# Kernel tuning notes

Hardware: AMD Instinct MI355X
Metric: run time of the kernel (lower is better)

Reference implementation:

```python
import jax, jax.numpy as jnp
import numpy as np

N_NEURONS = 50000
N_BKG = 100
N_SYN_BASIS = 5
N_EDGES = 500000
BATCH = 1
SEQ_T = 250
BKG_RATE_PROB = 0.25  # bkg_firing_rate(250) * 0.001


def setup_inputs() -> dict:
    key = jax.random.key(0)
    k_w, k_tau, k_sp, k_r, k_c = jax.random.split(key, 5)
    weights = jax.random.normal(k_w, (N_EDGES,), dtype=jnp.float32)
    tau_syn = jax.random.uniform(k_tau, (N_EDGES, N_SYN_BASIS), dtype=jnp.float32)
    # Bernoulli background spikes, shape [B*T, n_bkg_units]
    spikes = (jax.random.uniform(k_sp, (BATCH * SEQ_T, N_BKG)) < BKG_RATE_PROB).astype(jnp.float32)
    rows = jax.random.randint(k_r, (N_EDGES,), 0, N_NEURONS, dtype=jnp.int32)
    cols = jax.random.randint(k_c, (N_EDGES,), 0, N_BKG, dtype=jnp.int32)
    return {"weights": weights, "tau_syn": tau_syn, "spikes": spikes,
            "rows": rows, "cols": cols}


def reference(weights, tau_syn, spikes, rows, cols):
    # Per-receptor edge values: weights[e] * tau_syn[e, r]  -> [E, R]
    vals = weights[:, None] * tau_syn
    # Densify the (identical-structure) sparse matrix once for all receptors;
    # duplicate (row, col) indices accumulate, matching tf.sparse semantics
    # used through sparse_dense_matmul. W: [N, K, R]
    W = jnp.zeros((N_NEURONS, N_BKG, N_SYN_BASIS), dtype=spikes.dtype).at[rows, cols].add(vals)
    # i_receptor[r] = sparse_w_in @ spikes.T -> stacked [R, N, BT];
    # tf.transpose reverses axes -> [BT, N, R]; fused here as one einsum.
    out = jnp.einsum('nkr,bk->bnr', W, spikes)  # [BT, N, R]
    return out.reshape(BATCH, SEQ_T, N_NEURONS * N_SYN_BASIS)
```

## Files before the change

### kernel.cpp

```cpp
#include <hip/hip_runtime.h>


#define N_NEURONS 50000
#define N_BKG     100
#define N_SYN     5
#define N_EDGES   500000
#define SEQ_T     250
#define NCOL      (N_NEURONS * N_SYN)
#define RPB       16
#define NBINS     (N_NEURONS / RPB)
#define NPART     8
#define CAP_P     64
#define RECS_BIN  (NPART * CAP_P)
#define CPADF     80
#define BCOLS     80
#define STRIDE_J  37

#define LDS_BYTES 32000

#define WS_COUNT_OFF 0
#define WS_SPB_OFF   131072
#define WS_REC_OFF   262144

typedef __attribute__((ext_vector_type(8))) short bf16x8;
typedef __attribute__((ext_vector_type(4))) float f32x4;

__device__ inline unsigned short bf16_rne(float f) {
    unsigned u = __builtin_bit_cast(unsigned, f);
    u += 0x7FFFu + ((u >> 16) & 1u);
    return (unsigned short)(u >> 16);
}
__device__ inline float bf16_up(unsigned hw) {
    return __builtin_bit_cast(float, hw << 16);
}

__global__ __launch_bounds__(256) void bucket_kernel(
        const float* __restrict__ weights,
        const float* __restrict__ tau,
        const int*   __restrict__ rows,
        const int*   __restrict__ cols,
        const float* __restrict__ spikes,
        unsigned* __restrict__ count,
        uint4* __restrict__ rec,
        bf16x8* __restrict__ spbf) {
    int gid = blockIdx.x * 256 + threadIdx.x;
    if (gid < 4096) {
        int lane = gid & 63;
        int kk   = (gid >> 6) & 3;
        int nt   = gid >> 8;
        int t    = nt * 16 + (lane & 15);
        int k0   = kk * 32 + (lane >> 4) * 8;
        bf16x8 v;
#pragma unroll
        for (int i = 0; i < 8; ++i) {
            float s = 0.f;
            if (t < SEQ_T && (k0 + i) < N_BKG)
                s = spikes[t * N_BKG + k0 + i];
            v[i] = (short)bf16_rne(s);
        }
        spbf[gid] = v;
    }
    if (gid >= N_EDGES) return;
    int row = rows[gid];
    int col = cols[gid];
    float w = weights[gid];
    const float* tp = tau + (size_t)gid * N_SYN;
    int bin  = row >> 4;
    int part = blockIdx.x & (NPART - 1);
    unsigned slot = atomicAdd(&count[part * NBINS + bin], 1u);
    if (slot >= CAP_P) return;
    uint4 r;
    r.x = ((unsigned)col << 4) | (unsigned)(row & 15);
    r.y = (unsigned)bf16_rne(w * tp[0]) | ((unsigned)bf16_rne(w * tp[1]) << 16);
    r.z = (unsigned)bf16_rne(w * tp[2]) | ((unsigned)bf16_rne(w * tp[3]) << 16);
    r.w = (unsigned)bf16_rne(w * tp[4]);
    rec[(size_t)bin * RECS_BIN + part * CAP_P + slot] = r;
}

__global__ __launch_bounds__(256, 4) void fused_kernel(
        const unsigned* __restrict__ count,
        const uint4* __restrict__ rec,
        const bf16x8* __restrict__ spbf,
        float* __restrict__ out) {
    __shared__ __align__(16) char lds[LDS_BYTES];
    float* slice = (float*)lds;

    const int tid = threadIdx.x;
    const int l   = tid & 63;
    const int wv  = tid >> 6;
    const int lc  = l & 15;
    const int lq  = l >> 4;

    const int orig = blockIdx.x;
    const int xcd  = orig & 7;
    const int j    = orig >> 3;
    const int qx   = (xcd < 5) ? 391 : 390;
    const int base = (xcd < 5) ? xcd * 391 : 5 * 391 + (xcd - 5) * 390;
    const int bin  = base + (j * STRIDE_J) % qx;

    const uint4* rbin = rec + (size_t)bin * RECS_BIN;
    unsigned cntA = count[wv * NBINS + bin];
    unsigned cntB = count[(4 + wv) * NBINS + bin];
    if (cntA > CAP_P) cntA = CAP_P;
    if (cntB > CAP_P) cntB = CAP_P;
    uint4 ra = rbin[wv * CAP_P + l];
    uint4 rb = rbin[(4 + wv) * CAP_P + l];
    bool havea = (unsigned)l < cntA;
    bool haveb = (unsigned)l < cntB;

    {
        f32x4* s4 = (f32x4*)lds;
        f32x4 z = (f32x4){0.f, 0.f, 0.f, 0.f};
#pragma unroll
        for (int jj = 0; jj < 8; ++jj) {
            int i = tid + jj * 256;
            if (i < 2000) s4[i] = z;
        }
    }
    __syncthreads();

    if (havea) {
        float* bp = &slice[(ra.x >> 4) * CPADF + (ra.x & 15u) * N_SYN];
        atomicAdd(bp + 0, bf16_up(ra.y & 0xFFFFu));
        atomicAdd(bp + 1, bf16_up(ra.y >> 16));
        atomicAdd(bp + 2, bf16_up(ra.z & 0xFFFFu));
        atomicAdd(bp + 3, bf16_up(ra.z >> 16));
        atomicAdd(bp + 4, bf16_up(ra.w & 0xFFFFu));
    }
    if (haveb) {
        float* bp = &slice[(rb.x >> 4) * CPADF + (rb.x & 15u) * N_SYN];
        atomicAdd(bp + 0, bf16_up(rb.y & 0xFFFFu));
        atomicAdd(bp + 1, bf16_up(rb.y >> 16));
        atomicAdd(bp + 2, bf16_up(rb.z & 0xFFFFu));
        atomicAdd(bp + 3, bf16_up(rb.z >> 16));
        atomicAdd(bp + 4, bf16_up(rb.w & 0xFFFFu));
    }
    __syncthreads();

    bf16x8 hi[5];
#pragma unroll
    for (int jj = 0; jj < 5; ++jj) {
        int m  = tid + jj * 256;
        int c  = m % BCOLS;
        int kb = m / BCOLS;
#pragma unroll
        for (int i = 0; i < 8; ++i) {
            int k = kb * 8 + i;
            float v = (k < N_BKG) ? slice[k * CPADF + c] : 0.f;
            hi[jj][i] = (short)bf16_rne(v);
        }
    }
    __syncthreads();
#pragma unroll
    for (int jj = 0; jj < 5; ++jj) {
        int m  = tid + jj * 256;
        int c  = m % BCOLS;
        int kb = m / BCOLS;
        unsigned bo = (unsigned)(((c << 8) + (kb << 4)) ^ ((c & 7) << 4));
        *(bf16x8*)(lds + bo) = hi[jj];
    }

    bf16x8 bs[4][4];
#pragma unroll
    for (int n = 0; n < 4; ++n)
#pragma unroll
        for (int kk = 0; kk < 4; ++kk)
            bs[n][kk] = spbf[((wv * 4 + n) * 4 + kk) * 64 + l];
    __syncthreads();

    const size_t cb = (size_t)bin * BCOLS;
#pragma unroll
    for (int m = 0; m < 5; ++m) {
        f32x4 acc[4];
#pragma unroll
        for (int n = 0; n < 4; ++n)
            acc[n] = (f32x4){0.f, 0.f, 0.f, 0.f};

        int c = m * 16 + lc;
#pragma unroll
        for (int kk = 0; kk < 4; ++kk) {
            int bor = (((c << 8) + (kk << 6) + (lq << 4)) ^ ((c & 7) << 4));
            bf16x8 ah = *(const bf16x8*)(lds + bor);
#pragma unroll
            for (int n = 0; n < 4; ++n)
                acc[n] = __builtin_amdgcn_mfma_f32_16x16x32_bf16(
                             ah, bs[n][kk], acc[n], 0, 0, 0);
        }
        size_t cs = cb + m * 16 + lq * 4;
#pragma unroll
        for (int n = 0; n < 4; ++n) {
            int t = (wv * 4 + n) * 16 + lc;
            if (t < SEQ_T)
                *(f32x4*)(out + (size_t)t * NCOL + cs) = acc[n];
        }
    }
}

extern "C" void kernel_launch(void* const* d_in, const int* in_sizes, int n_in,
                              void* d_out, int out_size, void* d_ws, size_t ws_size,
                              hipStream_t stream) {
    const float* weights = (const float*)d_in[0];
    const float* tau     = (const float*)d_in[1];
    const float* spikes  = (const float*)d_in[2];
    const int*   rows    = (const int*)d_in[3];
    const int*   cols    = (const int*)d_in[4];
    float* out = (float*)d_out;

    char* ws = (char*)d_ws;
    unsigned* count = (unsigned*)(ws + WS_COUNT_OFF);
    bf16x8*   spbf  = (bf16x8*)(ws + WS_SPB_OFF);
    uint4*    rec   = (uint4*)(ws + WS_REC_OFF);

    hipMemsetAsync(count, 0, NPART * NBINS * sizeof(unsigned), stream);

    int eblocks = (N_EDGES + 255) / 256;
    bucket_kernel<<<eblocks, 256, 0, stream>>>(weights, tau, rows, cols, spikes,
                                               count, rec, spbf);

    fused_kernel<<<NBINS, 256, 0, stream>>>(count, rec, spbf, out);
}
```

Before: 112.6 us.

## Process two edges per thread, drop LDS bounds checks, pair M-tiles in MMA loop

The bucketing kernel now handles two edges per thread and launches half as many blocks. In the fused kernel, LDS grows to 40960 bytes so the zeroing and bf16 transpose reads run without bounds checks. The MFMA loop computes two 16-column tiles per pass, which gives more independent MFMA chains and groups the output stores. The costs are higher register pressure and more LDS per block, which may reduce occupancy. Also, because the loop interleaves edges, each bucketing block now mixes edges from two neighbouring groups of 256, which changes the partition assignment.

```diff
diff --git a/kernel.cpp b/kernel.cpp
--- a/kernel.cpp
+++ b/kernel.cpp
@@ -16,7 +16,7 @@
 #define BCOLS     80
 #define STRIDE_J  37
 
-#define LDS_BYTES 32000
+#define LDS_BYTES 40960
 
 #define WS_COUNT_OFF 0
 #define WS_SPB_OFF   131072
@@ -60,21 +60,25 @@
         }
         spbf[gid] = v;
     }
-    if (gid >= N_EDGES) return;
-    int row = rows[gid];
-    int col = cols[gid];
-    float w = weights[gid];
-    const float* tp = tau + (size_t)gid * N_SYN;
-    int bin  = row >> 4;
     int part = blockIdx.x & (NPART - 1);
-    unsigned slot = atomicAdd(&count[part * NBINS + bin], 1u);
-    if (slot >= CAP_P) return;
-    uint4 r;
-    r.x = ((unsigned)col << 4) | (unsigned)(row & 15);
-    r.y = (unsigned)bf16_rne(w * tp[0]) | ((unsigned)bf16_rne(w * tp[1]) << 16);
-    r.z = (unsigned)bf16_rne(w * tp[2]) | ((unsigned)bf16_rne(w * tp[3]) << 16);
-    r.w = (unsigned)bf16_rne(w * tp[4]);
-    rec[(size_t)bin * RECS_BIN + part * CAP_P + slot] = r;
+#pragma unroll
+    for (int u = 0; u < 2; ++u) {
+        int e = gid * 2 + u;
+        if (e >= N_EDGES) continue;
+        int row = rows[e];
+        int col = cols[e];
+        float w = weights[e];
+        const float* tp = tau + (size_t)e * N_SYN;
+        int bin = row >> 4;
+        unsigned slot = atomicAdd(&count[part * NBINS + bin], 1u);
+        if (slot >= CAP_P) continue;
+        uint4 r;
+        r.x = ((unsigned)col << 4) | (unsigned)(row & 15);
+        r.y = (unsigned)bf16_rne(w * tp[0]) | ((unsigned)bf16_rne(w * tp[1]) << 16);
+        r.z = (unsigned)bf16_rne(w * tp[2]) | ((unsigned)bf16_rne(w * tp[3]) << 16);
+        r.w = (unsigned)bf16_rne(w * tp[4]);
+        rec[(size_t)bin * RECS_BIN + part * CAP_P + slot] = r;
+    }
 }
 
 __global__ __launch_bounds__(256, 4) void fused_kernel(
@@ -112,10 +116,8 @@
         f32x4* s4 = (f32x4*)lds;
         f32x4 z = (f32x4){0.f, 0.f, 0.f, 0.f};
 #pragma unroll
-        for (int jj = 0; jj < 8; ++jj) {
-            int i = tid + jj * 256;
-            if (i < 2000) s4[i] = z;
-        }
+        for (int jj = 0; jj < 10; ++jj)
+            s4[tid + jj * 256] = z;
     }
     __syncthreads();
 
@@ -144,11 +146,8 @@
         int c  = m % BCOLS;
         int kb = m / BCOLS;
 #pragma unroll
-        for (int i = 0; i < 8; ++i) {
-            int k = kb * 8 + i;
-            float v = (k < N_BKG) ? slice[k * CPADF + c] : 0.f;
-            hi[jj][i] = (short)bf16_rne(v);
-        }
+        for (int i = 0; i < 8; ++i)
+            hi[jj][i] = (short)bf16_rne(slice[(kb * 8 + i) * CPADF + c]);
     }
     __syncthreads();
 #pragma unroll
@@ -170,28 +169,39 @@
 
     const size_t cb = (size_t)bin * BCOLS;
 #pragma unroll
-    for (int m = 0; m < 5; ++m) {
-        f32x4 acc[4];
-#pragma unroll
-        for (int n = 0; n < 4; ++n)
-            acc[n] = (f32x4){0.f, 0.f, 0.f, 0.f};
-
-        int c = m * 16 + lc;
-#pragma unroll
-        for (int kk = 0; kk < 4; ++kk) {
-            int bor = (((c << 8) + (kk << 6) + (lq << 4)) ^ ((c & 7) << 4));
-            bf16x8 ah = *(const bf16x8*)(lds + bor);
+    for (int mp = 0; mp < 3; ++mp) {
+        const int m0 = mp * 2;
+        const int nm = (mp < 2) ? 2 : 1;
+        f32x4 acc[2][4];
+#pragma unroll
+        for (int mi = 0; mi < 2; ++mi)
 #pragma unroll
             for (int n = 0; n < 4; ++n)
-                acc[n] = __builtin_amdgcn_mfma_f32_16x16x32_bf16(
-                             ah, bs[n][kk], acc[n], 0, 0, 0);
+                acc[mi][n] = (f32x4){0.f, 0.f, 0.f, 0.f};
+
+#pragma unroll
+        for (int mi = 0; mi < 2; ++mi) {
+            if (mi >= nm) break;
+            int c = (m0 + mi) * 16 + lc;
+#pragma unroll
+            for (int kk = 0; kk < 4; ++kk) {
+                int bor = (((c << 8) + (kk << 6) + (lq << 4)) ^ ((c & 7) << 4));
+                bf16x8 ah = *(const bf16x8*)(lds + bor);
+#pragma unroll
+                for (int n = 0; n < 4; ++n)
+                    acc[mi][n] = __builtin_amdgcn_mfma_f32_16x16x32_bf16(
+                                     ah, bs[n][kk], acc[mi][n], 0, 0, 0);
+            }
         }
-        size_t cs = cb + m * 16 + lq * 4;
 #pragma unroll
         for (int n = 0; n < 4; ++n) {
             int t = (wv * 4 + n) * 16 + lc;
-            if (t < SEQ_T)
-                *(f32x4*)(out + (size_t)t * NCOL + cs) = acc[n];
+            if (t < SEQ_T) {
+                float* op = out + (size_t)t * NCOL + cb + m0 * 16 + lq * 4;
+                *(f32x4*)op = acc[0][n];
+                if (nm > 1)
+                    *(f32x4*)(op + 16) = acc[1][n];
+            }
         }
     }
 }
@@ -213,7 +223,7 @@
 
     hipMemsetAsync(count, 0, NPART * NBINS * sizeof(unsigned), stream);
 
-    int eblocks = (N_EDGES + 255) / 256;
+    int eblocks = (N_EDGES / 2 + 255) / 256;
     bucket_kernel<<<eblocks, 256, 0, stream>>>(weights, tau, rows, cols, spikes,
                                                count, rec, spbf);
 
```

Result: faster. 104.5 us (-7.1%).
